# Kernel optimization log

Measured on AMD Instinct MI355X. Metric: run time of the kernel, lower is better.

The kernel has to match this reference:

```python
import jax, jax.numpy as jnp
import numpy as np

EPS = 1e-6

def _l2norm_axis1(x):
    # torch Normalize(2): divide by L2 norm over dim 1 (the T axis of [B,T,F])
    return x / jnp.sqrt(jnp.sum(x * x, axis=1, keepdims=True))

def _mlp(x, w1, b1, w2, b2):
    # frame_MLPEmbed / freq_MLPEmbed share structure: linear-relu-linear-l2norm(dim=1)
    h = jax.nn.relu(x @ w1 + b1)
    return _l2norm_axis1(h @ w2 + b2)

def _reshape_feat(f):
    # [L,B,C,T,D] -> permute(0,2,1,3) per layer -> [L,B,T,C*D]
    L, B, C, T, D = f.shape
    return jnp.transpose(f, (0, 1, 3, 2, 4)).reshape(L, B, T, C * D)

def _cos_time(x):
    # x: [L,B,T,C]; cosine sims between frames within each batch item -> [L,B,T,T]
    xn = x / (jnp.sqrt(jnp.sum(x * x, axis=-1, keepdims=True)) + EPS)
    S = (jnp.einsum('lbtc,lbsc->lbts', xn, xn) + 1.0) * 0.5
    return S / jnp.sum(S, axis=-1, keepdims=True)

def _cos_freq(x):
    # cosine sims between batch items per frame, returned as [L,B,T,B]
    xn = x / (jnp.sqrt(jnp.sum(x * x, axis=-1, keepdims=True)) + EPS)
    S = (jnp.einsum('lbtc,latc->lbta', xn, xn) + 1.0) * 0.5
    return S / jnp.sum(S, axis=-1, keepdims=True)

def _forward(feat_s, feat_t, tk_w1, tk_b1, tk_w2, tk_b2, fk_w1, fk_b1, fk_w2, fk_b2,
             tq_w1, tq_b1, tq_w2, tq_b2, fq_w1, fq_b1, fq_w2, fq_b2):
    feat_t = jax.lax.stop_gradient(feat_t)  # detach=True
    xs = _reshape_feat(feat_s)  # [s_len,B,T,CD]
    xt = _reshape_feat(feat_t)  # [t_len,B,T,CD]
    s_len, t_len = xs.shape[0], xt.shape[0]

    # gram matrices used for key/query MLPs
    sim_t = jnp.einsum('lbtc,lbsc->lbts', xt, xt)    # [t_len,B,T,T]
    sim_t_g = jnp.einsum('lbtc,latc->lbta', xt, xt)  # [t_len,B,T,B]
    sim_s = jnp.einsum('lbtc,lbsc->lbts', xs, xs)    # [s_len,B,T,T]
    sim_s_g = jnp.einsum('lbtc,latc->lbta', xs, xs)  # [s_len,B,T,B]

    mlp_v = jax.vmap(_mlp)  # vmap over the per-layer MLPs
    tk = mlp_v(sim_t, tk_w1, tk_b1, tk_w2, tk_b2)     # [t_len,B,T,T]
    fk = mlp_v(sim_t_g, fk_w1, fk_b1, fk_w2, fk_b2)   # [t_len,B,T,32]
    tq = mlp_v(sim_s, tq_w1, tq_b1, tq_w2, tq_b2)     # [s_len,B,T,T]
    fq = mlp_v(sim_s_g, fq_w1, fq_b1, fq_w2, fq_b2)   # [s_len,B,T,32]

    time_key = jnp.moveaxis(tk, 0, -1)    # [B,T,T,t_len]
    freq_key = jnp.moveaxis(fk, 0, -1)    # [B,T,32,t_len]
    time_query = jnp.moveaxis(tq, 0, 2)   # [B,T,s_len,T]
    freq_query = jnp.moveaxis(fq, 0, 2)   # [B,T,s_len,32]

    time_att = jax.nn.softmax(jnp.matmul(time_query, time_key), axis=-1)  # [B,T,s_len,t_len]
    freq_att = jax.nn.softmax(jnp.matmul(freq_query, freq_key), axis=-1)  # [B,T,s_len,t_len]

    stu_time = _cos_time(xs)  # [s_len,B,T,T]
    tea_time = _cos_time(xt)  # [t_len,B,T,T]
    stu_freq = _cos_freq(xs)  # [s_len,B,T,B]
    tea_freq = _cos_freq(xt)  # [t_len,B,T,B]

    # the torch nested lists are [i][j]; student entries depend only on i, teacher only on j
    stu_time_b = jnp.broadcast_to(stu_time[:, None], (s_len, t_len) + stu_time.shape[1:])
    stu_freq_b = jnp.broadcast_to(stu_freq[:, None], (s_len, t_len) + stu_freq.shape[1:])
    tea_time_b = jnp.broadcast_to(tea_time[None, :], (s_len, t_len) + tea_time.shape[1:])
    tea_freq_b = jnp.broadcast_to(tea_freq[None, :], (s_len, t_len) + tea_freq.shape[1:])

    return (stu_time_b, stu_freq_b, tea_time_b, tea_freq_b, time_att, freq_att)

def setup_inputs() -> dict:
    key = jax.random.key(0)
    ks = jax.random.split(key, 20)
    s_len, t_len, B, C, T, D = 4, 4, 8, 64, 256, 16
    H = 2 * T  # frame MLP hidden
    F = 32     # bsz * factor
    p = lambda k, shp: jax.random.normal(k, shp, dtype=jnp.float32) * 0.02
    return {
        'feat_s': jax.random.normal(ks[0], (s_len, B, C, T, D), dtype=jnp.float32),
        'feat_t': jax.random.normal(ks[1], (t_len, B, C, T, D), dtype=jnp.float32),
        'tk_w1': p(ks[2], (t_len, T, H)), 'tk_b1': p(ks[3], (t_len, H)),
        'tk_w2': p(ks[4], (t_len, H, T)), 'tk_b2': p(ks[5], (t_len, T)),
        'fk_w1': p(ks[6], (t_len, B, F)), 'fk_b1': p(ks[7], (t_len, F)),
        'fk_w2': p(ks[8], (t_len, F, F)), 'fk_b2': p(ks[9], (t_len, F)),
        'tq_w1': p(ks[10], (s_len, T, H)), 'tq_b1': p(ks[11], (s_len, H)),
        'tq_w2': p(ks[12], (s_len, H, T)), 'tq_b2': p(ks[13], (s_len, T)),
        'fq_w1': p(ks[14], (s_len, B, F)), 'fq_b1': p(ks[15], (s_len, F)),
        'fq_w2': p(ks[16], (s_len, F, F)), 'fq_b2': p(ks[17], (s_len, F)),
    }

def reference(feat_s, feat_t, tk_w1, tk_b1, tk_w2, tk_b2, fk_w1, fk_b1, fk_w2, fk_b2,
              tq_w1, tq_b1, tq_w2, tq_b2, fq_w1, fq_b1, fq_w2, fq_b2):
    return _forward(feat_s, feat_t, tk_w1, tk_b1, tk_w2, tk_b2, fk_w1, fk_b1, fk_w2, fk_b2,
                    tq_w1, tq_b1, tq_w2, tq_b2, fq_w1, fq_b1, fq_w2, fq_b2)
```

## Files before the change

### kernel.cpp

```cpp
#include <hip/hip_runtime.h>
#include <math.h>

typedef _Float16 half_t;
typedef _Float16 h2 __attribute__((ext_vector_type(2)));
typedef _Float16 h4 __attribute__((ext_vector_type(4)));
typedef _Float16 h8 __attribute__((ext_vector_type(8)));
typedef float f4 __attribute__((ext_vector_type(4)));
static constexpr float REPS = 1e-6f;

__global__ __launch_bounds__(256) void k_prep2(const float* __restrict__ tkw1, const float* __restrict__ tqw1,
                                               const float* __restrict__ tkw2, const float* __restrict__ tqw2,
                                               const float* __restrict__ tkb1, const float* __restrict__ tqb1,
                                               const float* __restrict__ tkb2, const float* __restrict__ tqb2,
                                               half_t* __restrict__ W1t, half_t* __restrict__ W2t,
                                               float* __restrict__ Bc1, float* __restrict__ Bc2,
                                               float* __restrict__ part,
                                               const float* __restrict__ fs, const float* __restrict__ ft,
                                               half_t* __restrict__ Xh, float* __restrict__ nrm) {
  __shared__ float T[64][65];
  int bid = blockIdx.x;
  int tid = threadIdx.x;
  if (bid < 256) {
    int z = bid >> 5, tile = bid & 31;
    int kt = tile >> 3, ntile = tile & 7;
    const float* src = (z < 4 ? tkw1 : tqw1) + (size_t)(z & 3) * 256 * 512;
#pragma unroll
    for (int q = 0; q < 16; q++) {
      int e = q * 256 + tid;
      int r = e >> 6, c = e & 63;
      T[r][c] = src[(size_t)(kt * 64 + r) * 512 + ntile * 64 + c];
    }
    __syncthreads();
#pragma unroll
    for (int q = 0; q < 16; q++) {
      int e = q * 256 + tid;
      int nn = e >> 6, kk = e & 63;
      W1t[(size_t)z * 512 * 256 + (size_t)(ntile * 64 + nn) * 256 + kt * 64 + kk] = (half_t)T[kk][nn];
    }
  } else if (bid < 512) {
    int bb = bid - 256;
    int z = bb >> 5, tile = bb & 31;
    int kt = tile >> 2, ntile = tile & 3;
    const float* src = (z < 4 ? tkw2 : tqw2) + (size_t)(z & 3) * 512 * 256;
#pragma unroll
    for (int q = 0; q < 16; q++) {
      int e = q * 256 + tid;
      int r = e >> 6, c = e & 63;
      T[r][c] = src[(size_t)(kt * 64 + r) * 256 + ntile * 64 + c];
    }
    __syncthreads();
#pragma unroll
    for (int q = 0; q < 16; q++) {
      int e = q * 256 + tid;
      int nn = e >> 6, kk = e & 63;
      W2t[(size_t)z * 256 * 512 + (size_t)(ntile * 64 + nn) * 512 + kt * 64 + kk] = (half_t)T[kk][nn];
    }
  } else if (bid == 512) {
    for (int e = tid; e < 4096; e += 256) {
      int z = e >> 9, n = e & 511;
      Bc1[e] = (z < 4 ? tkb1 : tqb1)[(z & 3) * 512 + n];
    }
    for (int e = tid; e < 2048; e += 256) {
      int z = e >> 8, n = e & 255;
      Bc2[e] = (z < 4 ? tkb2 : tqb2)[(z & 3) * 256 + n];
    }
    for (int e = tid; e < 16384; e += 256) part[e] = 0.f;
  } else {
    int bid2 = bid - 513;
    int tensor = bid2 >> 7;
    int l = (bid2 >> 5) & 3;
    int b = (bid2 >> 2) & 7;
    int tc = bid2 & 3;
    int tl = tid >> 2;
    int d0 = (tid & 3) * 4;
    int t = tc * 64 + tl;
    const float* base = (tensor ? ft : fs) + (size_t)((l * 8 + b) * 64) * 4096 + t * 16 + d0;
    size_t row = (size_t)(tensor * 32 + l * 8 + b) * 256 + t;
    half_t* xrow = Xh + row * 1024 + d0;
    float acc = 0.f;
#pragma unroll 8
    for (int c = 0; c < 64; c++) {
      float4 v = *(const float4*)(base + (size_t)c * 4096);
      acc += v.x * v.x + v.y * v.y + v.z * v.z + v.w * v.w;
      h4 hv;
      hv[0] = (half_t)v.x; hv[1] = (half_t)v.y; hv[2] = (half_t)v.z; hv[3] = (half_t)v.w;
      *(h4*)(xrow + c * 16) = hv;
    }
    acc += __shfl_xor(acc, 1);
    acc += __shfl_xor(acc, 2);
    if ((tid & 3) == 0) nrm[row] = sqrtf(acc);
  }
}

__global__ __launch_bounds__(256) void k_simg(const half_t* __restrict__ Xh,
                                              float* __restrict__ simg) {
  __shared__ __align__(16) half_t X[32 * 1032];
  int bid = blockIdx.x;
  int tensor = bid >> 8;
  int l = (bid >> 6) & 3;
  int tc = bid & 63;
  int t0 = tc * 4;
  int tid = threadIdx.x;
  {
    int r = tid >> 3, q = tid & 7;
    int b = r & 7, tl = r >> 3;
    const half_t* src = Xh + ((size_t)(tensor * 32 + l * 8 + b) * 256 + t0 + tl) * 1024;
    half_t* dst = X + (tl * 8 + b) * 1032;
    int c0 = q ^ (r & 7);
#pragma unroll
    for (int j = 0; j < 16; j++) {
      int c = c0 + 8 * j;
      *(h8*)(dst + c * 8) = *(const h8*)(src + c * 8);
    }
  }
  __syncthreads();
  int tl = tid >> 6;
  int ab = tid & 63;
  int b = ab >> 3, a = ab & 7;
  const half_t* xa = X + (tl * 8 + b) * 1032;
  const half_t* xb = X + (tl * 8 + a) * 1032;
  float acc = 0.f;
#pragma unroll 8
  for (int k = 0; k < 1024; k += 8) {
    h8 va = *(const h8*)(xa + k);
    h8 vb = *(const h8*)(xb + k);
#if __has_builtin(__builtin_amdgcn_fdot2)
#pragma unroll
    for (int i = 0; i < 4; i++) {
      h2 pa, pb;
      pa[0] = va[2 * i]; pa[1] = va[2 * i + 1];
      pb[0] = vb[2 * i]; pb[1] = vb[2 * i + 1];
      acc = __builtin_amdgcn_fdot2(pa, pb, acc, false);
    }
#else
#pragma unroll
    for (int e = 0; e < 8; e++) acc += (float)va[e] * (float)vb[e];
#endif
  }
  simg[(size_t)tensor * 65536 + ((size_t)(l * 8 + b) * 256 + t0 + tl) * 8 + a] = acc;
}

__global__ __launch_bounds__(512) void k_gram_cos(const half_t* __restrict__ Xh,
                                                  const float* __restrict__ nrm,
                                                  half_t* __restrict__ simh,
                                                  float* __restrict__ out_stu,
                                                  float* __restrict__ out_tea) {
  __shared__ __align__(16) half_t Bsm[256 * 64];
  __shared__ float rspart[64][4];
  __shared__ float rowsumS[64];
  int mt = blockIdx.x;
  int z = blockIdx.y;
  const half_t* Bb = Xh + (size_t)z * 256 * 1024;
  int tid = threadIdx.x;
  int w = tid >> 6, lane = tid & 63;
  int wm = w >> 2, wn = w & 3;
  int lr = lane & 15, lg = lane >> 4;
  f4 acc[2][4] = {};
  int r0 = tid >> 3, seg0 = tid & 7;
  int sw0 = (seg0 ^ (r0 & 7)) * 8;
  for (int kc = 0; kc < 1024; kc += 64) {
    h8 bv[4];
#pragma unroll
    for (int it = 0; it < 4; it++)
      bv[it] = *(const h8*)(Bb + (size_t)(it * 64 + r0) * 1024 + kc + seg0 * 8);
    __syncthreads();
#pragma unroll
    for (int it = 0; it < 4; it++)
      *(h8*)(Bsm + (it * 64 + r0) * 64 + sw0) = bv[it];
    __syncthreads();
#pragma unroll
    for (int kk = 0; kk < 2; kk++) {
      int g = kk * 4 + lg;
      h8 af[2], bf[4];
#pragma unroll
      for (int mf = 0; mf < 2; mf++) {
        int rA = mt * 64 + wm * 32 + mf * 16 + lr;
        af[mf] = *(const h8*)(Bsm + rA * 64 + ((g ^ (rA & 7)) * 8));
      }
#pragma unroll
      for (int nf = 0; nf < 4; nf++) {
        int rB = wn * 64 + nf * 16 + lr;
        bf[nf] = *(const h8*)(Bsm + rB * 64 + ((g ^ (rB & 7)) * 8));
      }
#pragma unroll
      for (int mf = 0; mf < 2; mf++)
#pragma unroll
        for (int nf = 0; nf < 4; nf++)
          acc[mf][nf] = __builtin_amdgcn_mfma_f32_16x16x32_f16(af[mf], bf[nf], acc[mf][nf], 0, 0, 0);
    }
  }
  int tensor = z >> 5, l = (z >> 3) & 3, b = z & 7;
  const float* nz = nrm + z * 256;
  float nc[4];
  int cols[4];
#pragma unroll
  for (int nf = 0; nf < 4; nf++) {
    cols[nf] = wn * 64 + nf * 16 + lr;
    nc[nf] = nz[cols[nf]] + REPS;
  }
  float v[2][4][4];
  float rowpart[2][4];
#pragma unroll
  for (int mf = 0; mf < 2; mf++) {
#pragma unroll
    for (int rg = 0; rg < 4; rg++) {
      int rib = wm * 32 + mf * 16 + lg * 4 + rg;
      float nr = nz[mt * 64 + rib] + REPS;
      float p = 0.f;
#pragma unroll
      for (int nf = 0; nf < 4; nf++) {
        float S = acc[mf][nf][rg];
        float vv = fmaf(S / (nr * nc[nf]), 0.5f, 0.5f);
        v[mf][nf][rg] = vv;
        p += vv;
        simh[(size_t)z * 65536 + (size_t)(mt * 64 + rib) * 256 + cols[nf]] = (half_t)S;
      }
      rowpart[mf][rg] = p;
    }
  }
#pragma unroll
  for (int mf = 0; mf < 2; mf++)
#pragma unroll
    for (int rg = 0; rg < 4; rg++) {
      float p = rowpart[mf][rg];
      p += __shfl_xor(p, 1); p += __shfl_xor(p, 2);
      p += __shfl_xor(p, 4); p += __shfl_xor(p, 8);
      rowpart[mf][rg] = p;
    }
  if (lr == 0) {
#pragma unroll
    for (int mf = 0; mf < 2; mf++)
#pragma unroll
      for (int rg = 0; rg < 4; rg++)
        rspart[wm * 32 + mf * 16 + lg * 4 + rg][wn] = rowpart[mf][rg];
  }
  __syncthreads();
  if (tid < 64)
    rowsumS[tid] = rspart[tid][0] + rspart[tid][1] + rspart[tid][2] + rspart[tid][3];
  __syncthreads();
  float* outp = tensor ? out_tea : out_stu;
#pragma unroll
  for (int mf = 0; mf < 2; mf++) {
#pragma unroll
    for (int rg = 0; rg < 4; rg++) {
      int rib = wm * 32 + mf * 16 + lg * 4 + rg;
      int t = mt * 64 + rib;
      float inv = 1.f / rowsumS[rib];
#pragma unroll
      for (int nf = 0; nf < 4; nf++) {
        float val = v[mf][nf][rg] * inv;
        size_t inner = ((size_t)(b * 256 + t)) * 256 + cols[nf];
        if (tensor == 0) {
          size_t base = (size_t)l * 4 * 524288;
#pragma unroll
          for (int j = 0; j < 4; j++) outp[base + (size_t)j * 524288 + inner] = val;
        } else {
#pragma unroll
          for (int i = 0; i < 4; i++) outp[((size_t)(i * 4 + l)) * 524288 + inner] = val;
        }
      }
    }
  }
}

template <int MODE, bool RELU, bool BIAS>
__global__ __launch_bounds__(256) void k_mfma(const half_t* __restrict__ A,
                                              const half_t* __restrict__ Bt,
                                              const float* __restrict__ bias,
                                              half_t* __restrict__ out,
                                              float* __restrict__ part) {
  constexpr int K = (MODE == 1) ? 256 : 512;
  constexpr int N = (MODE == 1) ? 512 : 256;
  __shared__ __align__(16) half_t Asm[128 * 64];
  __shared__ __align__(16) half_t Bsm[128 * 64];
  int z = blockIdx.z;
  size_t Aoff, Boff, Ooff;
  if (MODE == 1) {
    int l = z & 3, path = z >> 2;
    Aoff = ((size_t)((path == 0 ? 32 : 0) + l * 8)) * 256 * 256;
    Boff = (size_t)z * 512 * 256;
    Ooff = (size_t)z * 2048 * 512;
  } else {
    Aoff = (size_t)z * 2048 * 512; Boff = (size_t)z * 256 * 512; Ooff = (size_t)z * 2048 * 256;
  }
  const half_t* Ab = A + Aoff;
  const half_t* Bb = Bt + Boff;
  int mt = blockIdx.x, nt = blockIdx.y;
  int tid = threadIdx.x;
  int wave = tid >> 6, lane = tid & 63;
  int wm = (wave >> 1) * 64, wn = (wave & 1) * 64;
  int lr = lane & 15, lg = lane >> 4;
  f4 acc[4][4] = {};
  int r0 = tid >> 3, seg0 = tid & 7;
  int sw0 = (seg0 ^ (r0 & 7)) * 8;
  for (int kc = 0; kc < K; kc += 64) {
    h8 av[4], bv[4];
#pragma unroll
    for (int j = 0; j < 4; j++) {
      av[j] = *(const h8*)(Ab + (size_t)(mt * 128 + r0 + 32 * j) * K + kc + seg0 * 8);
      bv[j] = *(const h8*)(Bb + (size_t)(nt * 128 + r0 + 32 * j) * K + kc + seg0 * 8);
    }
    __syncthreads();
#pragma unroll
    for (int j = 0; j < 4; j++) {
      *(h8*)(Asm + (r0 + 32 * j) * 64 + sw0) = av[j];
      *(h8*)(Bsm + (r0 + 32 * j) * 64 + sw0) = bv[j];
    }
    __syncthreads();
#pragma unroll
    for (int kk = 0; kk < 2; kk++) {
      h8 af[4], bf[4];
#pragma unroll
      for (int mf = 0; mf < 4; mf++) {
        int r = wm + mf * 16 + lr;
        af[mf] = *(const h8*)(Asm + r * 64 + (((kk * 4 + lg) ^ (r & 7)) * 8));
      }
#pragma unroll
      for (int nf = 0; nf < 4; nf++) {
        int r = wn + nf * 16 + lr;
        bf[nf] = *(const h8*)(Bsm + r * 64 + (((kk * 4 + lg) ^ (r & 7)) * 8));
      }
#pragma unroll
      for (int mf = 0; mf < 4; mf++)
#pragma unroll
        for (int nf = 0; nf < 4; nf++)
          acc[mf][nf] = __builtin_amdgcn_mfma_f32_16x16x32_f16(af[mf], bf[nf], acc[mf][nf], 0, 0, 0);
    }
  }
  half_t* Ob = out + Ooff;
#pragma unroll
  for (int nf = 0; nf < 4; nf++) {
    int col = nt * 128 + wn + nf * 16 + lr;
    float bv2 = BIAS ? bias[z * N + col] : 0.f;
    float colsq = 0.f;
#pragma unroll
    for (int mf = 0; mf < 4; mf++) {
#pragma unroll
      for (int rg = 0; rg < 4; rg++) {
        int row = mt * 128 + wm + mf * 16 + lg * 4 + rg;
        float v = acc[mf][nf][rg] + bv2;
        if (RELU) v = fmaxf(v, 0.f);
        Ob[(size_t)row * N + col] = (half_t)v;
        if (MODE == 2) colsq += v * v;
      }
    }
    if (MODE == 2) {
      colsq += __shfl_xor(colsq, 16);
      colsq += __shfl_xor(colsq, 32);
      if (lg == 0) {
        int b = mt >> 1;
        atomicAdd(&part[((z * 8 + b) << 8) + col], colsq);
      }
    }
  }
}

__global__ __launch_bounds__(256) void k_small(const float* __restrict__ simg,
                                               const float* __restrict__ n,
                                               float* __restrict__ out_stu, float* __restrict__ out_tea,
                                               const float* __restrict__ qw1, const float* __restrict__ qb1,
                                               const float* __restrict__ qw2, const float* __restrict__ qb2,
                                               const float* __restrict__ kw1, const float* __restrict__ kb1,
                                               const float* __restrict__ kw2, const float* __restrict__ kb2,
                                               float* __restrict__ qout, float* __restrict__ kout) {
  __shared__ float sw1[8 * 32], sb1[32], sw2[32 * 32], sb2[32];
  __shared__ float zs[256][33];
  __shared__ float pcn[8][33];
  __shared__ float cn[32];
  int bid = blockIdx.x;
  int tid = threadIdx.x;
  if (bid < 64) {
    int tensor = bid >> 5;
    int lb = bid & 31;
    const float* sg = simg + (size_t)tensor * 65536;
    const float* nb2 = n + tensor * 8192;
    float* out = tensor ? out_tea : out_stu;
    int l = lb >> 3, b = lb & 7;
    int a = tid & 7;
    for (int tc = 0; tc < 8; tc++) {
      int t = tc * 32 + (tid >> 3);
      float nb = nb2[lb * 256 + t] + REPS;
      float na = nb2[(l * 8 + a) * 256 + t] + REPS;
      float v = (sg[((size_t)lb * 256 + t) * 8 + a] / (nb * na) + 1.f) * 0.5f;
      float w = v;
      for (int m = 1; m < 8; m <<= 1) w += __shfl_xor(w, m);
      v /= w;
      size_t inner = ((size_t)(b * 256 + t)) * 8 + a;
      if (tensor == 0) {
#pragma unroll
        for (int j = 0; j < 4; j++) out[((size_t)(l * 4 + j)) * 16384 + inner] = v;
      } else {
#pragma unroll
        for (int i = 0; i < 4; i++) out[((size_t)(i * 4 + l)) * 16384 + inner] = v;
      }
    }
  } else {
    int bb = bid - 64;
    int tensor = bb >> 5;
    int lb = bb & 31;
    int l = lb >> 3;
    const float* w1 = tensor ? kw1 : qw1;
    const float* b1 = tensor ? kb1 : qb1;
    const float* w2 = tensor ? kw2 : qw2;
    const float* b2 = tensor ? kb2 : qb2;
    const float* sg = simg + (size_t)tensor * 65536;
    float* outp = tensor ? kout : qout;
    int t = tid;
    sw1[t] = w1[l * 256 + t];
    if (t < 32) { sb1[t] = b1[l * 32 + t]; sb2[t] = b2[l * 32 + t]; }
    for (int q = t; q < 1024; q += 256) sw2[q] = w2[l * 1024 + q];
    __syncthreads();
    float x[8];
#pragma unroll
    for (int a = 0; a < 8; a++) x[a] = sg[((size_t)lb * 256 + t) * 8 + a];
    float h[32];
#pragma unroll
    for (int f = 0; f < 32; f++) {
      float acc = sb1[f];
#pragma unroll
      for (int a = 0; a < 8; a++) acc += x[a] * sw1[a * 32 + f];
      h[f] = fmaxf(acc, 0.f);
    }
#pragma unroll
    for (int g = 0; g < 32; g++) {
      float acc = sb2[g];
#pragma unroll
      for (int f = 0; f < 32; f++) acc += h[f] * sw2[f * 32 + g];
      zs[t][g] = acc;
    }
    __syncthreads();
    {
      int col = t & 31, ch = t >> 5;
      float sq = 0.f;
      for (int r = ch * 32; r < ch * 32 + 32; r++) { float v = zs[r][col]; sq += v * v; }
      pcn[ch][col] = sq;
    }
    __syncthreads();
    if (t < 32) {
      float ssum = 0.f;
#pragma unroll
      for (int c = 0; c < 8; c++) ssum += pcn[c][t];
      cn[t] = sqrtf(ssum);
    }
    __syncthreads();
#pragma unroll
    for (int g = 0; g < 32; g++)
      outp[((size_t)lb * 256 + t) * 32 + g] = zs[t][g] / cn[g];
  }
}

__global__ __launch_bounds__(64) void k_att(const half_t* __restrict__ Zq,
                                            const half_t* __restrict__ Zk,
                                            const float* __restrict__ part,
                                            const float* __restrict__ fq,
                                            const float* __restrict__ fk,
                                            float* __restrict__ out_time,
                                            float* __restrict__ out_freq) {
  int bid = blockIdx.x;
  int lane = threadIdx.x;
  if (bid < 2048) {
    int b = bid >> 8, t = bid & 255;
    float acc[4][4];
#pragma unroll
    for (int i = 0; i < 4; i++)
#pragma unroll
      for (int j = 0; j < 4; j++) acc[i][j] = 0.f;
    for (int it = 0; it < 4; it++) {
      int s = lane + it * 64;
      float qv[4], kv[4];
#pragma unroll
      for (int i = 0; i < 4; i++) {
        size_t lbO = (size_t)(i * 8 + b);
        float pq = part[(((4 + i) * 8 + b) << 8) + s];
        float pk = part[(((i) * 8 + b) << 8) + s];
        qv[i] = (float)Zq[(lbO * 256 + t) * 256 + s] * rsqrtf(pq);
        kv[i] = (float)Zk[(lbO * 256 + t) * 256 + s] * rsqrtf(pk);
      }
#pragma unroll
      for (int i = 0; i < 4; i++)
#pragma unroll
        for (int j = 0; j < 4; j++) acc[i][j] += qv[i] * kv[j];
    }
#pragma unroll
    for (int i = 0; i < 4; i++)
#pragma unroll
      for (int j = 0; j < 4; j++)
        for (int m = 32; m >= 1; m >>= 1) acc[i][j] += __shfl_xor(acc[i][j], m);
    if (lane < 16) {
      int i = lane >> 2, j = lane & 3;
      float mx = fmaxf(fmaxf(acc[i][0], acc[i][1]), fmaxf(acc[i][2], acc[i][3]));
      float sum = expf(acc[i][0] - mx) + expf(acc[i][1] - mx) + expf(acc[i][2] - mx) + expf(acc[i][3] - mx);
      out_time[(size_t)bid * 16 + lane] = expf(acc[i][j] - mx) / sum;
    }
  } else {
    int pair = bid - 2048;
    int b = pair >> 7, tp = pair & 127;
    int t = tp * 2 + (lane >> 5);
    int f = lane & 31;
    float qv[4], kv[4];
#pragma unroll
    for (int i = 0; i < 4; i++) {
      size_t lbO = (size_t)(i * 8 + b);
      qv[i] = fq[(lbO * 256 + t) * 32 + f];
      kv[i] = fk[(lbO * 256 + t) * 32 + f];
    }
    float acc[4][4];
#pragma unroll
    for (int i = 0; i < 4; i++)
#pragma unroll
      for (int j = 0; j < 4; j++) acc[i][j] = qv[i] * kv[j];
#pragma unroll
    for (int i = 0; i < 4; i++)
#pragma unroll
      for (int j = 0; j < 4; j++)
        for (int m = 16; m >= 1; m >>= 1) acc[i][j] += __shfl_xor(acc[i][j], m);
    int fl = lane & 31;
    if (fl < 16) {
      int i = fl >> 2, j = fl & 3;
      float mx = fmaxf(fmaxf(acc[i][0], acc[i][1]), fmaxf(acc[i][2], acc[i][3]));
      float sum = expf(acc[i][0] - mx) + expf(acc[i][1] - mx) + expf(acc[i][2] - mx) + expf(acc[i][3] - mx);
      out_freq[((size_t)(b * 256 + t)) * 16 + fl] = expf(acc[i][j] - mx) / sum;
    }
  }
}

extern "C" void kernel_launch(void* const* d_in, const int* in_sizes, int n_in,
                              void* d_out, int out_size, void* d_ws, size_t ws_size,
                              hipStream_t stream) {
  (void)in_sizes; (void)n_in; (void)out_size; (void)ws_size;
  const float* feat_s = (const float*)d_in[0];
  const float* feat_t = (const float*)d_in[1];
  const float* tk_w1 = (const float*)d_in[2];
  const float* tk_b1 = (const float*)d_in[3];
  const float* tk_w2 = (const float*)d_in[4];
  const float* tk_b2 = (const float*)d_in[5];
  const float* fk_w1 = (const float*)d_in[6];
  const float* fk_b1 = (const float*)d_in[7];
  const float* fk_w2 = (const float*)d_in[8];
  const float* fk_b2 = (const float*)d_in[9];
  const float* tq_w1 = (const float*)d_in[10];
  const float* tq_b1 = (const float*)d_in[11];
  const float* tq_w2 = (const float*)d_in[12];
  const float* tq_b2 = (const float*)d_in[13];
  const float* fq_w1 = (const float*)d_in[14];
  const float* fq_b1 = (const float*)d_in[15];
  const float* fq_w2 = (const float*)d_in[16];
  const float* fq_b2 = (const float*)d_in[17];

  float* ws = (float*)d_ws;
  half_t* Xh   = (half_t*)ws;
  half_t* hbuf = (half_t*)ws;
  half_t* Zbuf = (half_t*)(ws + 4194304);
  half_t* simh = (half_t*)(ws + 8388608);
  half_t* W1t  = (half_t*)(ws + 10485760);
  half_t* W2t  = (half_t*)(ws + 11010048);
  float* Bc1   = ws + 11534336;
  float* Bc2   = ws + 11538432;
  float* simg  = ws + 11540480;
  float* nrm   = ws + 11671552;
  float* part  = ws + 11687936;
  float* fkb   = ws + 11704320;
  float* fqb   = ws + 11966464;

  float* out = (float*)d_out;
  float* out_stu_time = out;
  float* out_stu_freq = out + 8388608;
  float* out_tea_time = out + 8650752;
  float* out_tea_freq = out + 17039360;
  float* out_time_att = out + 17301504;
  float* out_freq_att = out + 17334272;

  hipLaunchKernelGGL(k_prep2, dim3(769), dim3(256), 0, stream,
                     tk_w1, tq_w1, tk_w2, tq_w2, tk_b1, tq_b1, tk_b2, tq_b2,
                     W1t, W2t, Bc1, Bc2, part, feat_s, feat_t, Xh, nrm);
  hipLaunchKernelGGL(k_simg, dim3(512), dim3(256), 0, stream, Xh, simg);
  hipLaunchKernelGGL(k_gram_cos, dim3(4, 64), dim3(512), 0, stream,
                     Xh, nrm, simh, out_stu_time, out_tea_time);
  hipLaunchKernelGGL(k_small, dim3(128), dim3(256), 0, stream, simg, nrm,
                     out_stu_freq, out_tea_freq,
                     fq_w1, fq_b1, fq_w2, fq_b2, fk_w1, fk_b1, fk_w2, fk_b2, fqb, fkb);
  hipLaunchKernelGGL((k_mfma<1, true, true>), dim3(16, 4, 8), dim3(256), 0, stream,
                     simh, W1t, Bc1, hbuf, (float*)nullptr);
  hipLaunchKernelGGL((k_mfma<2, false, true>), dim3(16, 2, 8), dim3(256), 0, stream,
                     hbuf, W2t, Bc2, Zbuf, part);
  hipLaunchKernelGGL(k_att, dim3(3072), dim3(64), 0, stream,
                     Zbuf + (size_t)4 * 2048 * 256, Zbuf, part, fqb, fkb,
                     out_time_att, out_freq_att);
}
```

Baseline: 129.8 us.

## Merge independent kernels into combined launches to cut launch count

```diff
diff --git a/kernel.cpp b/kernel.cpp
--- a/kernel.cpp
+++ b/kernel.cpp
@@ -92,286 +92,258 @@
   }
 }
 
-__global__ __launch_bounds__(256) void k_simg(const half_t* __restrict__ Xh,
-                                              float* __restrict__ simg) {
-  __shared__ __align__(16) half_t X[32 * 1032];
+__global__ __launch_bounds__(512) void k_gs(const half_t* __restrict__ Xh,
+                                            const float* __restrict__ nrm,
+                                            half_t* __restrict__ simh,
+                                            float* __restrict__ out_stu,
+                                            float* __restrict__ out_tea,
+                                            float* __restrict__ simg) {
+  __shared__ __align__(16) char smem[66048];
   int bid = blockIdx.x;
-  int tensor = bid >> 8;
-  int l = (bid >> 6) & 3;
-  int tc = bid & 63;
-  int t0 = tc * 4;
   int tid = threadIdx.x;
-  {
-    int r = tid >> 3, q = tid & 7;
-    int b = r & 7, tl = r >> 3;
-    const half_t* src = Xh + ((size_t)(tensor * 32 + l * 8 + b) * 256 + t0 + tl) * 1024;
-    half_t* dst = X + (tl * 8 + b) * 1032;
-    int c0 = q ^ (r & 7);
-#pragma unroll
-    for (int j = 0; j < 16; j++) {
-      int c = c0 + 8 * j;
-      *(h8*)(dst + c * 8) = *(const h8*)(src + c * 8);
-    }
-  }
-  __syncthreads();
-  int tl = tid >> 6;
-  int ab = tid & 63;
-  int b = ab >> 3, a = ab & 7;
-  const half_t* xa = X + (tl * 8 + b) * 1032;
-  const half_t* xb = X + (tl * 8 + a) * 1032;
-  float acc = 0.f;
+  if (bid < 256) {
+    half_t* Bsm = (half_t*)smem;
+    float* rspart = (float*)(smem + 32768);
+    float* rowsumS = (float*)(smem + 32768 + 1024);
+    int mt = bid & 3;
+    int z = bid >> 2;
+    const half_t* Bb = Xh + (size_t)z * 256 * 1024;
+    int w = tid >> 6, lane = tid & 63;
+    int wm = w >> 2, wn = w & 3;
+    int lr = lane & 15, lg = lane >> 4;
+    f4 acc[2][4] = {};
+    int r0 = tid >> 3, seg0 = tid & 7;
+    int sw0 = (seg0 ^ (r0 & 7)) * 8;
+    for (int kc = 0; kc < 1024; kc += 64) {
+      h8 bv[4];
+#pragma unroll
+      for (int it = 0; it < 4; it++)
+        bv[it] = *(const h8*)(Bb + (size_t)(it * 64 + r0) * 1024 + kc + seg0 * 8);
+      __syncthreads();
+#pragma unroll
+      for (int it = 0; it < 4; it++)
+        *(h8*)(Bsm + (it * 64 + r0) * 64 + sw0) = bv[it];
+      __syncthreads();
+#pragma unroll
+      for (int kk = 0; kk < 2; kk++) {
+        int g = kk * 4 + lg;
+        h8 af[2], bf[4];
+#pragma unroll
+        for (int mf = 0; mf < 2; mf++) {
+          int rA = mt * 64 + wm * 32 + mf * 16 + lr;
+          af[mf] = *(const h8*)(Bsm + rA * 64 + ((g ^ (rA & 7)) * 8));
+        }
+#pragma unroll
+        for (int nf = 0; nf < 4; nf++) {
+          int rB = wn * 64 + nf * 16 + lr;
+          bf[nf] = *(const h8*)(Bsm + rB * 64 + ((g ^ (rB & 7)) * 8));
+        }
+#pragma unroll
+        for (int mf = 0; mf < 2; mf++)
+#pragma unroll
+          for (int nf = 0; nf < 4; nf++)
+            acc[mf][nf] = __builtin_amdgcn_mfma_f32_16x16x32_f16(af[mf], bf[nf], acc[mf][nf], 0, 0, 0);
+      }
+    }
+    int tensor = z >> 5, l = (z >> 3) & 3, b = z & 7;
+    const float* nz = nrm + z * 256;
+    float nc[4];
+    int cols[4];
+#pragma unroll
+    for (int nf = 0; nf < 4; nf++) {
+      cols[nf] = wn * 64 + nf * 16 + lr;
+      nc[nf] = nz[cols[nf]] + REPS;
+    }
+    float v[2][4][4];
+    float rowpart[2][4];
+#pragma unroll
+    for (int mf = 0; mf < 2; mf++) {
+#pragma unroll
+      for (int rg = 0; rg < 4; rg++) {
+        int rib = wm * 32 + mf * 16 + lg * 4 + rg;
+        float nr = nz[mt * 64 + rib] + REPS;
+        float p = 0.f;
+#pragma unroll
+        for (int nf = 0; nf < 4; nf++) {
+          float S = acc[mf][nf][rg];
+          float vv = fmaf(S / (nr * nc[nf]), 0.5f, 0.5f);
+          v[mf][nf][rg] = vv;
+          p += vv;
+          simh[(size_t)z * 65536 + (size_t)(mt * 64 + rib) * 256 + cols[nf]] = (half_t)S;
+        }
+        rowpart[mf][rg] = p;
+      }
+    }
+#pragma unroll
+    for (int mf = 0; mf < 2; mf++)
+#pragma unroll
+      for (int rg = 0; rg < 4; rg++) {
+        float p = rowpart[mf][rg];
+        p += __shfl_xor(p, 1); p += __shfl_xor(p, 2);
+        p += __shfl_xor(p, 4); p += __shfl_xor(p, 8);
+        rowpart[mf][rg] = p;
+      }
+    if (lr == 0) {
+#pragma unroll
+      for (int mf = 0; mf < 2; mf++)
+#pragma unroll
+        for (int rg = 0; rg < 4; rg++)
+          rspart[(wm * 32 + mf * 16 + lg * 4 + rg) * 4 + wn] = rowpart[mf][rg];
+    }
+    __syncthreads();
+    if (tid < 64)
+      rowsumS[tid] = rspart[tid * 4] + rspart[tid * 4 + 1] + rspart[tid * 4 + 2] + rspart[tid * 4 + 3];
+    __syncthreads();
+    float* outp = tensor ? out_tea : out_stu;
+#pragma unroll
+    for (int mf = 0; mf < 2; mf++) {
+#pragma unroll
+      for (int rg = 0; rg < 4; rg++) {
+        int rib = wm * 32 + mf * 16 + lg * 4 + rg;
+        int t = mt * 64 + rib;
+        float inv = 1.f / rowsumS[rib];
+#pragma unroll
+        for (int nf = 0; nf < 4; nf++) {
+          float val = v[mf][nf][rg] * inv;
+          size_t inner = ((size_t)(b * 256 + t)) * 256 + cols[nf];
+          if (tensor == 0) {
+            size_t base = (size_t)l * 4 * 524288;
+#pragma unroll
+            for (int j = 0; j < 4; j++) outp[base + (size_t)j * 524288 + inner] = val;
+          } else {
+#pragma unroll
+            for (int i = 0; i < 4; i++) outp[((size_t)(i * 4 + l)) * 524288 + inner] = val;
+          }
+        }
+      }
+    }
+  } else {
+    half_t* X = (half_t*)smem;
+    int sb = bid - 256;
+    int tensor = sb >> 8;
+    int l = (sb >> 6) & 3;
+    int tc = sb & 63;
+    int t0 = tc * 4;
+#pragma unroll
+    for (int j = 0; j < 8; j++) {
+      int i = j * 512 + tid;
+      int r = i >> 7, col = i & 127;
+      int b = r & 7, tl = r >> 3;
+      const half_t* src = Xh + ((size_t)(tensor * 32 + l * 8 + b) * 256 + t0 + tl) * 1024 + col * 8;
+      *(h8*)(X + r * 1032 + col * 8) = *(const h8*)src;
+    }
+    __syncthreads();
+    if (tid < 256) {
+      int tl = tid >> 6;
+      int ab = tid & 63;
+      int b = ab >> 3, a = ab & 7;
+      const half_t* xa = X + (tl * 8 + b) * 1032;
+      const half_t* xb = X + (tl * 8 + a) * 1032;
+      float acc = 0.f;
 #pragma unroll 8
-  for (int k = 0; k < 1024; k += 8) {
-    h8 va = *(const h8*)(xa + k);
-    h8 vb = *(const h8*)(xb + k);
+      for (int k = 0; k < 1024; k += 8) {
+        h8 va = *(const h8*)(xa + k);
+        h8 vb = *(const h8*)(xb + k);
 #if __has_builtin(__builtin_amdgcn_fdot2)
 #pragma unroll
-    for (int i = 0; i < 4; i++) {
-      h2 pa, pb;
-      pa[0] = va[2 * i]; pa[1] = va[2 * i + 1];
-      pb[0] = vb[2 * i]; pb[1] = vb[2 * i + 1];
-      acc = __builtin_amdgcn_fdot2(pa, pb, acc, false);
-    }
+        for (int i = 0; i < 4; i++) {
+          h2 pa, pb;
+          pa[0] = va[2 * i]; pa[1] = va[2 * i + 1];
+          pb[0] = vb[2 * i]; pb[1] = vb[2 * i + 1];
+          acc = __builtin_amdgcn_fdot2(pa, pb, acc, false);
+        }
 #else
 #pragma unroll
-    for (int e = 0; e < 8; e++) acc += (float)va[e] * (float)vb[e];
+        for (int e = 0; e < 8; e++) acc += (float)va[e] * (float)vb[e];
 #endif
-  }
-  simg[(size_t)tensor * 65536 + ((size_t)(l * 8 + b) * 256 + t0 + tl) * 8 + a] = acc;
-}
-
-__global__ __launch_bounds__(512) void k_gram_cos(const half_t* __restrict__ Xh,
-                                                  const float* __restrict__ nrm,
-                                                  half_t* __restrict__ simh,
-                                                  float* __restrict__ out_stu,
-                                                  float* __restrict__ out_tea) {
-  __shared__ __align__(16) half_t Bsm[256 * 64];
-  __shared__ float rspart[64][4];
-  __shared__ float rowsumS[64];
-  int mt = blockIdx.x;
-  int z = blockIdx.y;
-  const half_t* Bb = Xh + (size_t)z * 256 * 1024;
-  int tid = threadIdx.x;
-  int w = tid >> 6, lane = tid & 63;
-  int wm = w >> 2, wn = w & 3;
-  int lr = lane & 15, lg = lane >> 4;
-  f4 acc[2][4] = {};
-  int r0 = tid >> 3, seg0 = tid & 7;
-  int sw0 = (seg0 ^ (r0 & 7)) * 8;
-  for (int kc = 0; kc < 1024; kc += 64) {
-    h8 bv[4];
-#pragma unroll
-    for (int it = 0; it < 4; it++)
-      bv[it] = *(const h8*)(Bb + (size_t)(it * 64 + r0) * 1024 + kc + seg0 * 8);
-    __syncthreads();
-#pragma unroll
-    for (int it = 0; it < 4; it++)
-      *(h8*)(Bsm + (it * 64 + r0) * 64 + sw0) = bv[it];
-    __syncthreads();
-#pragma unroll
-    for (int kk = 0; kk < 2; kk++) {
-      int g = kk * 4 + lg;
-      h8 af[2], bf[4];
-#pragma unroll
-      for (int mf = 0; mf < 2; mf++) {
-        int rA = mt * 64 + wm * 32 + mf * 16 + lr;
-        af[mf] = *(const h8*)(Bsm + rA * 64 + ((g ^ (rA & 7)) * 8));
-      }
-#pragma unroll
-      for (int nf = 0; nf < 4; nf++) {
-        int rB = wn * 64 + nf * 16 + lr;
-        bf[nf] = *(const h8*)(Bsm + rB * 64 + ((g ^ (rB & 7)) * 8));
-      }
-#pragma unroll
-      for (int mf = 0; mf < 2; mf++)
-#pragma unroll
-        for (int nf = 0; nf < 4; nf++)
-          acc[mf][nf] = __builtin_amdgcn_mfma_f32_16x16x32_f16(af[mf], bf[nf], acc[mf][nf], 0, 0, 0);
-    }
-  }
-  int tensor = z >> 5, l = (z >> 3) & 3, b = z & 7;
-  const float* nz = nrm + z * 256;
-  float nc[4];
-  int cols[4];
-#pragma unroll
-  for (int nf = 0; nf < 4; nf++) {
-    cols[nf] = wn * 64 + nf * 16 + lr;
-    nc[nf] = nz[cols[nf]] + REPS;
-  }
-  float v[2][4][4];
-  float rowpart[2][4];
-#pragma unroll
-  for (int mf = 0; mf < 2; mf++) {
-#pragma unroll
-    for (int rg = 0; rg < 4; rg++) {
-      int rib = wm * 32 + mf * 16 + lg * 4 + rg;
-      float nr = nz[mt * 64 + rib] + REPS;
-      float p = 0.f;
-#pragma unroll
-      for (int nf = 0; nf < 4; nf++) {
-        float S = acc[mf][nf][rg];
-        float vv = fmaf(S / (nr * nc[nf]), 0.5f, 0.5f);
-        v[mf][nf][rg] = vv;
-        p += vv;
-        simh[(size_t)z * 65536 + (size_t)(mt * 64 + rib) * 256 + cols[nf]] = (half_t)S;
-      }
-      rowpart[mf][rg] = p;
-    }
-  }
-#pragma unroll
-  for (int mf = 0; mf < 2; mf++)
-#pragma unroll
-    for (int rg = 0; rg < 4; rg++) {
-      float p = rowpart[mf][rg];
-      p += __shfl_xor(p, 1); p += __shfl_xor(p, 2);
-      p += __shfl_xor(p, 4); p += __shfl_xor(p, 8);
-      rowpart[mf][rg] = p;
-    }
-  if (lr == 0) {
-#pragma unroll
-    for (int mf = 0; mf < 2; mf++)
-#pragma unroll
-      for (int rg = 0; rg < 4; rg++)
-        rspart[wm * 32 + mf * 16 + lg * 4 + rg][wn] = rowpart[mf][rg];
-  }
-  __syncthreads();
-  if (tid < 64)
-    rowsumS[tid] = rspart[tid][0] + rspart[tid][1] + rspart[tid][2] + rspart[tid][3];
-  __syncthreads();
-  float* outp = tensor ? out_tea : out_stu;
-#pragma unroll
-  for (int mf = 0; mf < 2; mf++) {
-#pragma unroll
-    for (int rg = 0; rg < 4; rg++) {
-      int rib = wm * 32 + mf * 16 + lg * 4 + rg;
-      int t = mt * 64 + rib;
-      float inv = 1.f / rowsumS[rib];
-#pragma unroll
-      for (int nf = 0; nf < 4; nf++) {
-        float val = v[mf][nf][rg] * inv;
-        size_t inner = ((size_t)(b * 256 + t)) * 256 + cols[nf];
-        if (tensor == 0) {
-          size_t base = (size_t)l * 4 * 524288;
-#pragma unroll
-          for (int j = 0; j < 4; j++) outp[base + (size_t)j * 524288 + inner] = val;
-        } else {
-#pragma unroll
-          for (int i = 0; i < 4; i++) outp[((size_t)(i * 4 + l)) * 524288 + inner] = val;
-        }
-      }
+      }
+      simg[(size_t)tensor * 65536 + ((size_t)(l * 8 + b) * 256 + t0 + tl) * 8 + a] = acc;
     }
   }
 }
 
-template <int MODE, bool RELU, bool BIAS>
-__global__ __launch_bounds__(256) void k_mfma(const half_t* __restrict__ A,
-                                              const half_t* __restrict__ Bt,
-                                              const float* __restrict__ bias,
-                                              half_t* __restrict__ out,
-                                              float* __restrict__ part) {
-  constexpr int K = (MODE == 1) ? 256 : 512;
-  constexpr int N = (MODE == 1) ? 512 : 256;
-  __shared__ __align__(16) half_t Asm[128 * 64];
-  __shared__ __align__(16) half_t Bsm[128 * 64];
-  int z = blockIdx.z;
-  size_t Aoff, Boff, Ooff;
-  if (MODE == 1) {
-    int l = z & 3, path = z >> 2;
-    Aoff = ((size_t)((path == 0 ? 32 : 0) + l * 8)) * 256 * 256;
-    Boff = (size_t)z * 512 * 256;
-    Ooff = (size_t)z * 2048 * 512;
-  } else {
-    Aoff = (size_t)z * 2048 * 512; Boff = (size_t)z * 256 * 512; Ooff = (size_t)z * 2048 * 256;
-  }
-  const half_t* Ab = A + Aoff;
-  const half_t* Bb = Bt + Boff;
-  int mt = blockIdx.x, nt = blockIdx.y;
-  int tid = threadIdx.x;
-  int wave = tid >> 6, lane = tid & 63;
-  int wm = (wave >> 1) * 64, wn = (wave & 1) * 64;
-  int lr = lane & 15, lg = lane >> 4;
-  f4 acc[4][4] = {};
-  int r0 = tid >> 3, seg0 = tid & 7;
-  int sw0 = (seg0 ^ (r0 & 7)) * 8;
-  for (int kc = 0; kc < K; kc += 64) {
-    h8 av[4], bv[4];
-#pragma unroll
-    for (int j = 0; j < 4; j++) {
-      av[j] = *(const h8*)(Ab + (size_t)(mt * 128 + r0 + 32 * j) * K + kc + seg0 * 8);
-      bv[j] = *(const h8*)(Bb + (size_t)(nt * 128 + r0 + 32 * j) * K + kc + seg0 * 8);
-    }
-    __syncthreads();
-#pragma unroll
-    for (int j = 0; j < 4; j++) {
-      *(h8*)(Asm + (r0 + 32 * j) * 64 + sw0) = av[j];
-      *(h8*)(Bsm + (r0 + 32 * j) * 64 + sw0) = bv[j];
-    }
-    __syncthreads();
-#pragma unroll
-    for (int kk = 0; kk < 2; kk++) {
-      h8 af[4], bf[4];
-#pragma unroll
-      for (int mf = 0; mf < 4; mf++) {
-        int r = wm + mf * 16 + lr;
-        af[mf] = *(const h8*)(Asm + r * 64 + (((kk * 4 + lg) ^ (r & 7)) * 8));
-      }
-#pragma unroll
-      for (int nf = 0; nf < 4; nf++) {
-        int r = wn + nf * 16 + lr;
-        bf[nf] = *(const h8*)(Bsm + r * 64 + (((kk * 4 + lg) ^ (r & 7)) * 8));
-      }
-#pragma unroll
-      for (int mf = 0; mf < 4; mf++)
-#pragma unroll
-        for (int nf = 0; nf < 4; nf++)
-          acc[mf][nf] = __builtin_amdgcn_mfma_f32_16x16x32_f16(af[mf], bf[nf], acc[mf][nf], 0, 0, 0);
-    }
-  }
-  half_t* Ob = out + Ooff;
-#pragma unroll
-  for (int nf = 0; nf < 4; nf++) {
-    int col = nt * 128 + wn + nf * 16 + lr;
-    float bv2 = BIAS ? bias[z * N + col] : 0.f;
-    float colsq = 0.f;
-#pragma unroll
-    for (int mf = 0; mf < 4; mf++) {
-#pragma unroll
-      for (int rg = 0; rg < 4; rg++) {
-        int row = mt * 128 + wm + mf * 16 + lg * 4 + rg;
-        float v = acc[mf][nf][rg] + bv2;
-        if (RELU) v = fmaxf(v, 0.f);
-        Ob[(size_t)row * N + col] = (half_t)v;
-        if (MODE == 2) colsq += v * v;
-      }
-    }
-    if (MODE == 2) {
-      colsq += __shfl_xor(colsq, 16);
-      colsq += __shfl_xor(colsq, 32);
-      if (lg == 0) {
-        int b = mt >> 1;
-        atomicAdd(&part[((z * 8 + b) << 8) + col], colsq);
-      }
-    }
-  }
-}
-
-__global__ __launch_bounds__(256) void k_small(const float* __restrict__ simg,
-                                               const float* __restrict__ n,
-                                               float* __restrict__ out_stu, float* __restrict__ out_tea,
-                                               const float* __restrict__ qw1, const float* __restrict__ qb1,
-                                               const float* __restrict__ qw2, const float* __restrict__ qb2,
-                                               const float* __restrict__ kw1, const float* __restrict__ kb1,
-                                               const float* __restrict__ kw2, const float* __restrict__ kb2,
-                                               float* __restrict__ qout, float* __restrict__ kout) {
-  __shared__ float sw1[8 * 32], sb1[32], sw2[32 * 32], sb2[32];
-  __shared__ float zs[256][33];
-  __shared__ float pcn[8][33];
-  __shared__ float cn[32];
+__global__ __launch_bounds__(256) void k_m1s(const half_t* __restrict__ simh,
+                                             const half_t* __restrict__ W1t,
+                                             const float* __restrict__ Bc1,
+                                             half_t* __restrict__ hbuf,
+                                             const float* __restrict__ simg,
+                                             const float* __restrict__ n,
+                                             float* __restrict__ out_stu, float* __restrict__ out_tea,
+                                             const float* __restrict__ qw1, const float* __restrict__ qb1,
+                                             const float* __restrict__ qw2, const float* __restrict__ qb2,
+                                             const float* __restrict__ kw1, const float* __restrict__ kb1,
+                                             const float* __restrict__ kw2, const float* __restrict__ kb2,
+                                             float* __restrict__ qout, float* __restrict__ kout) {
+  __shared__ __align__(16) char smem[40352];
   int bid = blockIdx.x;
   int tid = threadIdx.x;
-  if (bid < 64) {
-    int tensor = bid >> 5;
-    int lb = bid & 31;
+  if (bid < 512) {
+    constexpr int K = 256, N = 512;
+    half_t* Asm = (half_t*)smem;
+    half_t* Bsm = (half_t*)(smem + 16384);
+    int mt = bid & 15, nt = (bid >> 4) & 3, z = bid >> 6;
+    int l = z & 3, path = z >> 2;
+    const half_t* Ab = simh + ((size_t)((path == 0 ? 32 : 0) + l * 8)) * 256 * 256;
+    const half_t* Bb = W1t + (size_t)z * 512 * 256;
+    half_t* Ob = hbuf + (size_t)z * 2048 * 512;
+    int wave = tid >> 6, lane = tid & 63;
+    int wm = (wave >> 1) * 64, wn = (wave & 1) * 64;
+    int lr = lane & 15, lg = lane >> 4;
+    f4 acc[4][4] = {};
+    int r0 = tid >> 3, seg0 = tid & 7;
+    int sw0 = (seg0 ^ (r0 & 7)) * 8;
+    for (int kc = 0; kc < K; kc += 64) {
+      h8 av[4], bv[4];
+#pragma unroll
+      for (int j = 0; j < 4; j++) {
+        av[j] = *(const h8*)(Ab + (size_t)(mt * 128 + r0 + 32 * j) * K + kc + seg0 * 8);
+        bv[j] = *(const h8*)(Bb + (size_t)(nt * 128 + r0 + 32 * j) * K + kc + seg0 * 8);
+      }
+      __syncthreads();
+#pragma unroll
+      for (int j = 0; j < 4; j++) {
+        *(h8*)(Asm + (r0 + 32 * j) * 64 + sw0) = av[j];
+        *(h8*)(Bsm + (r0 + 32 * j) * 64 + sw0) = bv[j];
+      }
+      __syncthreads();
+#pragma unroll
+      for (int kk = 0; kk < 2; kk++) {
+        h8 af[4], bf[4];
+#pragma unroll
+        for (int mf = 0; mf < 4; mf++) {
+          int r = wm + mf * 16 + lr;
+          af[mf] = *(const h8*)(Asm + r * 64 + (((kk * 4 + lg) ^ (r & 7)) * 8));
+        }
+#pragma unroll
+        for (int nf = 0; nf < 4; nf++) {
+          int r = wn + nf * 16 + lr;
+          bf[nf] = *(const h8*)(Bsm + r * 64 + (((kk * 4 + lg) ^ (r & 7)) * 8));
+        }
+#pragma unroll
+        for (int mf = 0; mf < 4; mf++)
+#pragma unroll
+          for (int nf = 0; nf < 4; nf++)
+            acc[mf][nf] = __builtin_amdgcn_mfma_f32_16x16x32_f16(af[mf], bf[nf], acc[mf][nf], 0, 0, 0);
+      }
+    }
+#pragma unroll
+    for (int nf = 0; nf < 4; nf++) {
+      int col = nt * 128 + wn + nf * 16 + lr;
+      float bv2 = Bc1[z * N + col];
+#pragma unroll
+      for (int mf = 0; mf < 4; mf++) {
+#pragma unroll
+        for (int rg = 0; rg < 4; rg++) {
+          int row = mt * 128 + wm + mf * 16 + lg * 4 + rg;
+          float v = fmaxf(acc[mf][nf][rg] + bv2, 0.f);
+          Ob[(size_t)row * N + col] = (half_t)v;
+        }
+      }
+    }
+  } else if (bid < 576) {
+    int bb = bid - 512;
+    int tensor = bb >> 5;
+    int lb = bb & 31;
     const float* sg = simg + (size_t)tensor * 65536;
     const float* nb2 = n + tensor * 8192;
     float* out = tensor ? out_tea : out_stu;
@@ -395,7 +367,14 @@
       }
     }
   } else {
-    int bb = bid - 64;
+    float* sw1 = (float*)smem;
+    float* sb1 = (float*)(smem + 1024);
+    float* sw2 = (float*)(smem + 1152);
+    float* sb2 = (float*)(smem + 5248);
+    float* zs  = (float*)(smem + 5376);
+    float* pcn = (float*)(smem + 39168);
+    float* cn  = (float*)(smem + 40224);
+    int bb = bid - 576;
     int tensor = bb >> 5;
     int lb = bb & 31;
     int l = lb >> 3;
@@ -426,26 +405,104 @@
       float acc = sb2[g];
 #pragma unroll
       for (int f = 0; f < 32; f++) acc += h[f] * sw2[f * 32 + g];
-      zs[t][g] = acc;
+      zs[t * 33 + g] = acc;
     }
     __syncthreads();
     {
       int col = t & 31, ch = t >> 5;
       float sq = 0.f;
-      for (int r = ch * 32; r < ch * 32 + 32; r++) { float v = zs[r][col]; sq += v * v; }
-      pcn[ch][col] = sq;
+      for (int r = ch * 32; r < ch * 32 + 32; r++) { float v = zs[r * 33 + col]; sq += v * v; }
+      pcn[ch * 33 + col] = sq;
     }
     __syncthreads();
     if (t < 32) {
       float ssum = 0.f;
 #pragma unroll
-      for (int c = 0; c < 8; c++) ssum += pcn[c][t];
+      for (int c = 0; c < 8; c++) ssum += pcn[c * 33 + t];
       cn[t] = sqrtf(ssum);
     }
     __syncthreads();
 #pragma unroll
     for (int g = 0; g < 32; g++)
-      outp[((size_t)lb * 256 + t) * 32 + g] = zs[t][g] / cn[g];
+      outp[((size_t)lb * 256 + t) * 32 + g] = zs[t * 33 + g] / cn[g];
+  }
+}
+
+__global__ __launch_bounds__(256) void k_mfma2(const half_t* __restrict__ A,
+                                               const half_t* __restrict__ Bt,
+                                               const float* __restrict__ bias,
+                                               half_t* __restrict__ out,
+                                               float* __restrict__ part) {
+  constexpr int K = 512, N = 256;
+  __shared__ __align__(16) half_t Asm[128 * 64];
+  __shared__ __align__(16) half_t Bsm[128 * 64];
+  int z = blockIdx.z;
+  const half_t* Ab = A + (size_t)z * 2048 * 512;
+  const half_t* Bb = Bt + (size_t)z * 256 * 512;
+  half_t* Ob = out + (size_t)z * 2048 * 256;
+  int mt = blockIdx.x, nt = blockIdx.y;
+  int tid = threadIdx.x;
+  int wave = tid >> 6, lane = tid & 63;
+  int wm = (wave >> 1) * 64, wn = (wave & 1) * 64;
+  int lr = lane & 15, lg = lane >> 4;
+  f4 acc[4][4] = {};
+  int r0 = tid >> 3, seg0 = tid & 7;
+  int sw0 = (seg0 ^ (r0 & 7)) * 8;
+  for (int kc = 0; kc < K; kc += 64) {
+    h8 av[4], bv[4];
+#pragma unroll
+    for (int j = 0; j < 4; j++) {
+      av[j] = *(const h8*)(Ab + (size_t)(mt * 128 + r0 + 32 * j) * K + kc + seg0 * 8);
+      bv[j] = *(const h8*)(Bb + (size_t)(nt * 128 + r0 + 32 * j) * K + kc + seg0 * 8);
+    }
+    __syncthreads();
+#pragma unroll
+    for (int j = 0; j < 4; j++) {
+      *(h8*)(Asm + (r0 + 32 * j) * 64 + sw0) = av[j];
+      *(h8*)(Bsm + (r0 + 32 * j) * 64 + sw0) = bv[j];
+    }
+    __syncthreads();
+#pragma unroll
+    for (int kk = 0; kk < 2; kk++) {
+      h8 af[4], bf[4];
+#pragma unroll
+      for (int mf = 0; mf < 4; mf++) {
+        int r = wm + mf * 16 + lr;
+        af[mf] = *(const h8*)(Asm + r * 64 + (((kk * 4 + lg) ^ (r & 7)) * 8));
+      }
+#pragma unroll
+      for (int nf = 0; nf < 4; nf++) {
+        int r = wn + nf * 16 + lr;
+        bf[nf] = *(const h8*)(Bsm + r * 64 + (((kk * 4 + lg) ^ (r & 7)) * 8));
+      }
+#pragma unroll
+      for (int mf = 0; mf < 4; mf++)
+#pragma unroll
+        for (int nf = 0; nf < 4; nf++)
+          acc[mf][nf] = __builtin_amdgcn_mfma_f32_16x16x32_f16(af[mf], bf[nf], acc[mf][nf], 0, 0, 0);
+    }
+  }
+#pragma unroll
+  for (int nf = 0; nf < 4; nf++) {
+    int col = nt * 128 + wn + nf * 16 + lr;
+    float bv2 = bias[z * N + col];
+    float colsq = 0.f;
+#pragma unroll
+    for (int mf = 0; mf < 4; mf++) {
+#pragma unroll
+      for (int rg = 0; rg < 4; rg++) {
+        int row = mt * 128 + wm + mf * 16 + lg * 4 + rg;
+        float v = acc[mf][nf][rg] + bv2;
+        Ob[(size_t)row * N + col] = (half_t)v;
+        colsq += v * v;
+      }
+    }
+    colsq += __shfl_xor(colsq, 16);
+    colsq += __shfl_xor(colsq, 32);
+    if (lg == 0) {
+      int b = mt >> 1;
+      atomicAdd(&part[((z * 8 + b) << 8) + col], colsq);
+    }
   }
 }
 
@@ -573,15 +630,13 @@
   hipLaunchKernelGGL(k_prep2, dim3(769), dim3(256), 0, stream,
                      tk_w1, tq_w1, tk_w2, tq_w2, tk_b1, tq_b1, tk_b2, tq_b2,
                      W1t, W2t, Bc1, Bc2, part, feat_s, feat_t, Xh, nrm);
-  hipLaunchKernelGGL(k_simg, dim3(512), dim3(256), 0, stream, Xh, simg);
-  hipLaunchKernelGGL(k_gram_cos, dim3(4, 64), dim3(512), 0, stream,
-                     Xh, nrm, simh, out_stu_time, out_tea_time);
-  hipLaunchKernelGGL(k_small, dim3(128), dim3(256), 0, stream, simg, nrm,
+  hipLaunchKernelGGL(k_gs, dim3(768), dim3(512), 0, stream,
+                     Xh, nrm, simh, out_stu_time, out_tea_time, simg);
+  hipLaunchKernelGGL(k_m1s, dim3(640), dim3(256), 0, stream,
+                     simh, W1t, Bc1, hbuf, simg, nrm,
                      out_stu_freq, out_tea_freq,
                      fq_w1, fq_b1, fq_w2, fq_b2, fk_w1, fk_b1, fk_w2, fk_b2, fqb, fkb);
-  hipLaunchKernelGGL((k_mfma<1, true, true>), dim3(16, 4, 8), dim3(256), 0, stream,
-                     simh, W1t, Bc1, hbuf, (float*)nullptr);
-  hipLaunchKernelGGL((k_mfma<2, false, true>), dim3(16, 2, 8), dim3(256), 0, stream,
+  hipLaunchKernelGGL(k_mfma2, dim3(16, 2, 8), dim3(256), 0, stream,
                      hbuf, W2t, Bc2, Zbuf, part);
   hipLaunchKernelGGL(k_att, dim3(3072), dim3(64), 0, stream,
                      Zbuf + (size_t)4 * 2048 * 256, Zbuf, part, fqb, fkb,
```

After: 124.2 us. -4.3%, faster.
